# Kernel optimization log

Hardware: AMD Instinct MI355X
Metric: run time of the kernel (lower is better)

The kernel has to match this reference:

```python
import jax, jax.numpy as jnp
import numpy as np


def setup_inputs() -> dict:
    key = jax.random.key(0)
    k1, k2 = jax.random.split(key)
    B, D, T = 8, 256, 4096
    Q, K = 8, 1024
    z = jax.random.normal(k1, (B, D, T), dtype=jnp.float32)
    # original init: uniform(-1/n_e, 1/n_e)
    codebooks = jax.random.uniform(k2, (Q, K, D), dtype=jnp.float32,
                                   minval=-1.0 / K, maxval=1.0 / K)
    return {"z": z, "codebooks": codebooks}


def reference(z, codebooks):
    # z: [B, e_dim, T]; codebooks: [Q, n_e, e_dim]
    zp = jnp.transpose(z, (0, 2, 1))  # [B, T, D]
    residual = zp
    quantized_out = jnp.zeros_like(zp)
    total_loss = jnp.zeros((), dtype=z.dtype)
    all_indices = []
    Q = codebooks.shape[0]
    for q in range(Q):  # small fixed number of residual stages
        E = codebooks[q]  # [K, D]
        # squared euclidean distances: ||r||^2 + ||e||^2 - 2 r.e
        d = (jnp.sum(residual ** 2, axis=-1, keepdims=True)
             + jnp.sum(E ** 2, axis=-1)
             - 2.0 * jnp.einsum('btd,kd->btk', residual, E))  # [B, T, K]
        idx = jnp.argmin(d, axis=-1)  # [B, T]
        z_q = E[idx]                  # [B, T, D] gather
        loss = (jnp.mean((jax.lax.stop_gradient(z_q) - residual) ** 2)
                + 0.25 * jnp.mean((z_q - jax.lax.stop_gradient(residual)) ** 2))
        # straight-through estimator
        z_q_st = residual + jax.lax.stop_gradient(z_q - residual)
        residual = residual - z_q_st
        quantized_out = quantized_out + z_q_st
        total_loss = total_loss + loss
        all_indices.append(idx)
    quantized_out = jnp.transpose(quantized_out, (0, 2, 1))  # [B, D, T]
    return quantized_out, total_loss, jnp.stack(all_indices)  # indices: [Q, B, T]
```

## Files before the change

kernel.cpp:

```cpp
#include <hip/hip_runtime.h>

#define B_   8
#define D_   256
#define T_   4096
#define Q_   8
#define K_   1024
#define BT_  (B_*T_)
#define N_   (B_*T_*D_)
#define LOSS_OFF N_
#define IDX_OFF  (N_+1)
#define ROWS 32

typedef __attribute__((ext_vector_type(8))) short short8;
typedef __attribute__((ext_vector_type(4))) float float4v;

union U4S8 { uint4 u; short8 s; };

__device__ __forceinline__ unsigned short f2bf(float x) {
    unsigned int u = __float_as_uint(x);
    unsigned int r = (u + 0x7FFFu + ((u >> 16) & 1u)) >> 16;
    return (unsigned short)r;
}
__device__ __forceinline__ float bf2f(unsigned short b) {
    return __uint_as_float(((unsigned int)b) << 16);
}
__device__ __forceinline__ unsigned fkey(float f) {
    unsigned u = __float_as_uint(f);
    return (u & 0x80000000u) ? ~u : (u | 0x80000000u);
}
__device__ __forceinline__ float fkeyinv(unsigned k) {
    unsigned u = (k & 0x80000000u) ? (k & 0x7fffffffu) : ~k;
    return __uint_as_float(u);
}


__global__ void k_init(const float* __restrict__ z, float* __restrict__ residual,
                       double* lossAcc) {
    __shared__ float tile[32][33];
    int b  = blockIdx.z;
    int d0 = blockIdx.y * 32;
    int t0 = blockIdx.x * 32;
    int tx = threadIdx.x & 31;
    int ty = threadIdx.x >> 5;
    const float* zb = z + (size_t)b * D_ * T_;
    #pragma unroll
    for (int r = 0; r < 32; r += 8)
        tile[ty + r][tx] = zb[(size_t)(d0 + ty + r) * T_ + t0 + tx];
    __syncthreads();
    float* rb = residual + (size_t)b * T_ * D_;
    #pragma unroll
    for (int r = 0; r < 32; r += 8)
        rb[(size_t)(t0 + ty + r) * D_ + d0 + tx] = tile[tx][ty + r];
    if (b == 0 && blockIdx.x == 0 && blockIdx.y == 0 && threadIdx.x == 0)
        *lossAcc = 0.0;
}


__global__ void k_bfrag(const float* __restrict__ cb, uint4* __restrict__ Bfrag) {
    int gid = blockIdx.x * 256 + threadIdx.x;
    int q    = gid >> 15;
    int rem  = gid & 32767;
    int ct   = rem >> 9;
    int kc   = (rem >> 6) & 7;
    int lane = rem & 63;
    int cand = ct * 16 + (lane & 15);
    int kb   = kc * 32 + (lane >> 4) * 8;
    const float* e = cb + ((size_t)q * K_ + cand) * D_ + kb;
    float4v u0 = *(const float4v*)(e);
    float4v u1 = *(const float4v*)(e + 4);
    float vv[8] = {u0.x, u0.y, u0.z, u0.w, u1.x, u1.y, u1.z, u1.w};
    unsigned short h[8], l[8];
    #pragma unroll
    for (int j = 0; j < 8; ++j) {
        float v = vv[j];
        h[j] = f2bf(v);
        l[j] = f2bf(v - bf2f(h[j]));
    }
    uint4 hi, lo;
    hi.x = (unsigned)h[0] | ((unsigned)h[1] << 16);
    hi.y = (unsigned)h[2] | ((unsigned)h[3] << 16);
    hi.z = (unsigned)h[4] | ((unsigned)h[5] << 16);
    hi.w = (unsigned)h[6] | ((unsigned)h[7] << 16);
    lo.x = (unsigned)l[0] | ((unsigned)l[1] << 16);
    lo.y = (unsigned)l[2] | ((unsigned)l[3] << 16);
    lo.z = (unsigned)l[4] | ((unsigned)l[5] << 16);
    lo.w = (unsigned)l[6] | ((unsigned)l[7] << 16);
    size_t base = (((size_t)(q * 64 + ct) * 8 + kc) * 2) * 64;
    Bfrag[base + lane]      = hi;
    Bfrag[base + 64 + lane] = lo;
}


__global__ void k_se(const float* __restrict__ cb, float* __restrict__ Se) {
    int gid = blockIdx.x * 256 + threadIdx.x;
    int i  = gid >> 4;
    int ln = gid & 15;
    if (i >= Q_ * K_) return;
    const float* e = cb + (size_t)i * D_ + ln * 16;
    float4v v0 = *(const float4v*)(e);
    float4v v1 = *(const float4v*)(e + 4);
    float4v v2 = *(const float4v*)(e + 8);
    float4v v3 = *(const float4v*)(e + 12);
    float vv[16] = {v0.x, v0.y, v0.z, v0.w, v1.x, v1.y, v1.z, v1.w,
                    v2.x, v2.y, v2.z, v2.w, v3.x, v3.y, v3.z, v3.w};
    double s = 0.0;
    #pragma unroll
    for (int d = 0; d < 16; ++d) {
        float a = vv[d] * vv[d];
        s += (double)a;
    }
    #pragma unroll
    for (int st = 8; st > 0; st >>= 1) s += __shfl_xor(s, st);
    if (ln == 0) Se[i] = (float)s;
}


__launch_bounds__(512, 2)
__global__ void k_stage(const float* __restrict__ cb,
                        const uint4* __restrict__ Bfrag,
                        const float* __restrict__ Se,
                        float* __restrict__ residual,
                        float* __restrict__ out,
                        double* __restrict__ lossAcc,
                        int q) {
    __shared__ union {
        uint4 afr[2048];
        struct { int slist[32][16]; float sdd[32][16];
                 int srow[512]; int sslot[512]; } post;
        struct { float ovd[512]; int ovk[512]; } over;
        double lred[8];
    } sc;
    __shared__ float seL[1024];
    __shared__ float srb[32], margin[32];
    __shared__ unsigned sminI[32];
    __shared__ int   scount[32], sidx[32];
    __shared__ int   nSurv;

    const int tid  = threadIdx.x;
    const int lane = tid & 63;
    const int w    = tid >> 6;
    const int quad = lane >> 4;
    const int lc   = lane & 15;
    const int row0 = blockIdx.x * ROWS;
    const int g    = tid >> 8;
    const int dt   = tid & 255;

    if (tid < 32) { scount[tid] = 0; sminI[tid] = 0xFFFFFFFFu; }
    if (tid == 32) nSurv = 0;
    seL[tid]       = Se[q * K_ + tid];
    seL[tid + 512] = Se[q * K_ + tid + 512];

    const uint4* __restrict__ Bq = Bfrag + (size_t)q * (64 * 8 * 2 * 64);
    U4S8 b0h, b0l, b1h, b1l;
    {
        const uint4* p0 = Bq + (((size_t)((w * 8 + 0) * 8 + 0)) * 2) * 64 + lane;
        b0h.u = p0[0]; b0l.u = p0[64];
        const uint4* p1 = Bq + (((size_t)((w * 8 + 1) * 8 + 0)) * 2) * 64 + lane;
        b1h.u = p1[0]; b1l.u = p1[64];
    }

    {
        int row = tid >> 4, seg = tid & 15;
        int rg = row >> 4, rlo = row & 15;
        int kc = seg >> 1, par = seg & 1;
        const float* rp = residual + (size_t)(row0 + row) * D_ + seg * 16;
        float4v v0 = *(const float4v*)(rp);
        float4v v1 = *(const float4v*)(rp + 4);
        float4v v2 = *(const float4v*)(rp + 8);
        float4v v3 = *(const float4v*)(rp + 12);
        float vv[16] = {v0.x, v0.y, v0.z, v0.w, v1.x, v1.y, v1.z, v1.w,
                        v2.x, v2.y, v2.z, v2.w, v3.x, v3.y, v3.z, v3.w};
        double s = 0.0; float sa = 0.0f;
        #pragma unroll
        for (int i = 0; i < 16; ++i) {
            float v = vv[i];
            s += (double)(v * v);
            sa += fabsf(v);
        }
        #pragma unroll
        for (int st = 8; st > 0; st >>= 1) {
            s  += __shfl_xor(s, st);
            sa += __shfl_xor(sa, st);
        }
        if (seg == 0) {
            float sr = (float)s;
            float sb = sa * 1.001f;
            srb[row]    = sr;
            margin[row] = 9.6e-7f * sr + 4.0e-7f * sb + 2.0e-4f;
        }
        #pragma unroll
        for (int h = 0; h < 2; ++h) {
            unsigned short hh[8], ll[8];
            #pragma unroll
            for (int j = 0; j < 8; ++j) {
                float v = vv[h * 8 + j];
                hh[j] = f2bf(v);
                ll[j] = f2bf(v - bf2f(hh[j]));
            }
            uint4 hiW, loW;
            hiW.x = (unsigned)hh[0] | ((unsigned)hh[1] << 16);
            hiW.y = (unsigned)hh[2] | ((unsigned)hh[3] << 16);
            hiW.z = (unsigned)hh[4] | ((unsigned)hh[5] << 16);
            hiW.w = (unsigned)hh[6] | ((unsigned)hh[7] << 16);
            loW.x = (unsigned)ll[0] | ((unsigned)ll[1] << 16);
            loW.y = (unsigned)ll[2] | ((unsigned)ll[3] << 16);
            loW.z = (unsigned)ll[4] | ((unsigned)ll[5] << 16);
            loW.w = (unsigned)ll[6] | ((unsigned)ll[7] << 16);
            int ln = (par * 2 + h) * 16 + rlo;
            int sl = ln ^ kc;
            sc.afr[((rg * 8 + kc) * 2 + 0) * 64 + sl] = hiW;
            sc.afr[((rg * 8 + kc) * 2 + 1) * 64 + sl] = loW;
        }
    }
    __syncthreads();

    float4v accA[16];
    #pragma unroll
    for (int i = 0; i < 16; ++i) accA[i] = (float4v){0.f, 0.f, 0.f, 0.f};

    for (int kc = 0; kc < 8; ++kc) {
        U4S8 a0h, a0l, a1h, a1l;
        a0h.u = sc.afr[((0 * 8 + kc) * 2 + 0) * 64 + (lane ^ kc)];
        a0l.u = sc.afr[((0 * 8 + kc) * 2 + 1) * 64 + (lane ^ kc)];
        a1h.u = sc.afr[((1 * 8 + kc) * 2 + 0) * 64 + (lane ^ kc)];
        a1l.u = sc.afr[((1 * 8 + kc) * 2 + 1) * 64 + (lane ^ kc)];
        #pragma unroll
        for (int ctl = 0; ctl < 8; ++ctl) {
            U4S8 bh, bl;
            if ((ctl & 1) == 0) { bh = b0h; bl = b0l; }
            else                { bh = b1h; bl = b1l; }
            {
                int pkc  = kc + ((ctl + 2) >> 3);
                int pctl = (ctl + 2) & 7;
                const uint4* p = Bq + (((size_t)((w * 8 + pctl) * 8 + pkc)) * 2) * 64 + lane;
                if ((ctl & 1) == 0) { b0h.u = p[0]; b0l.u = p[64]; }
                else                { b1h.u = p[0]; b1l.u = p[64]; }
            }
            float4v a0 = accA[ctl * 2 + 0];
            a0 = __builtin_amdgcn_mfma_f32_16x16x32_bf16(a0h.s, bh.s, a0, 0, 0, 0);
            a0 = __builtin_amdgcn_mfma_f32_16x16x32_bf16(a0l.s, bh.s, a0, 0, 0, 0);
            a0 = __builtin_amdgcn_mfma_f32_16x16x32_bf16(a0h.s, bl.s, a0, 0, 0, 0);
            accA[ctl * 2 + 0] = a0;
            float4v a1 = accA[ctl * 2 + 1];
            a1 = __builtin_amdgcn_mfma_f32_16x16x32_bf16(a1h.s, bh.s, a1, 0, 0, 0);
            a1 = __builtin_amdgcn_mfma_f32_16x16x32_bf16(a1l.s, bh.s, a1, 0, 0, 0);
            a1 = __builtin_amdgcn_mfma_f32_16x16x32_bf16(a1h.s, bl.s, a1, 0, 0, 0);
            accA[ctl * 2 + 1] = a1;
        }
    }

    float sr8[8];
    #pragma unroll
    for (int rr = 0; rr < 8; ++rr)
        sr8[rr] = srb[(rr >> 2) * 16 + quad * 4 + (rr & 3)];

    float mn[8];
    #pragma unroll
    for (int rr = 0; rr < 8; ++rr) mn[rr] = 3.4e38f;
    #pragma unroll
    for (int ctl = 0; ctl < 8; ++ctl) {
        int cand = (w * 8 + ctl) * 16 + lc;
        float se = seL[cand];
        #pragma unroll
        for (int rr = 0; rr < 8; ++rr) {
            float dd = (sr8[rr] + se) - 2.0f * accA[ctl * 2 + (rr >> 2)][rr & 3];
            mn[rr] = fminf(mn[rr], dd);
        }
    }
    #pragma unroll
    for (int rr = 0; rr < 8; ++rr) {
        float v = mn[rr];
        v = fminf(v, __shfl_xor(v, 1));
        v = fminf(v, __shfl_xor(v, 2));
        v = fminf(v, __shfl_xor(v, 4));
        v = fminf(v, __shfl_xor(v, 8));
        if (lc == 0)
            atomicMin(&sminI[(rr >> 2) * 16 + quad * 4 + (rr & 3)], fkey(v));
    }
    __syncthreads();

    float thrV[8];
    #pragma unroll
    for (int rr = 0; rr < 8; ++rr) {
        int row = (rr >> 2) * 16 + quad * 4 + (rr & 3);
        thrV[rr] = fkeyinv(sminI[row]) + margin[row];
    }
    #pragma unroll
    for (int ctl = 0; ctl < 8; ++ctl) {
        int cand = (w * 8 + ctl) * 16 + lc;
        float se = seL[cand];
        #pragma unroll
        for (int rr = 0; rr < 8; ++rr) {
            int row = (rr >> 2) * 16 + quad * 4 + (rr & 3);
            float dd = (sr8[rr] + se) - 2.0f * accA[ctl * 2 + (rr >> 2)][rr & 3];
            if (dd <= thrV[rr]) {
                int p = atomicAdd(&scount[row], 1);
                if (p < 16) sc.post.slist[row][p] = cand;
            }
        }
    }
    __syncthreads();

    if (tid < 32) {
        int cnt = scount[tid];
        if (cnt == 1) {
            sidx[tid] = sc.post.slist[tid][0];
        } else if (cnt >= 2 && cnt <= 16) {
            int base = atomicAdd(&nSurv, cnt);
            for (int s2 = 0; s2 < cnt; ++s2) {
                sc.post.srow[base + s2]  = tid;
                sc.post.sslot[base + s2] = s2;
            }
        }
    }
    __syncthreads();

    {
        int nS  = nSurv;
        int grp = tid >> 4, ln = tid & 15;
        for (int j = grp; j < nS; j += 32) {
            int row  = sc.post.srow[j];
            int slot = sc.post.sslot[j];
            int k    = sc.post.slist[row][slot];
            const float* Ek = cb + ((size_t)q * K_ + k) * D_ + ln * 16;
            const float* Rk = residual + (size_t)(row0 + row) * D_ + ln * 16;
            float4v e0 = *(const float4v*)(Ek);
            float4v e1 = *(const float4v*)(Ek + 4);
            float4v e2 = *(const float4v*)(Ek + 8);
            float4v e3 = *(const float4v*)(Ek + 12);
            float4v r0 = *(const float4v*)(Rk);
            float4v r1 = *(const float4v*)(Rk + 4);
            float4v r2 = *(const float4v*)(Rk + 8);
            float4v r3 = *(const float4v*)(Rk + 12);
            float ev[16] = {e0.x, e0.y, e0.z, e0.w, e1.x, e1.y, e1.z, e1.w,
                            e2.x, e2.y, e2.z, e2.w, e3.x, e3.y, e3.z, e3.w};
            float rv2[16] = {r0.x, r0.y, r0.z, r0.w, r1.x, r1.y, r1.z, r1.w,
                             r2.x, r2.y, r2.z, r2.w, r3.x, r3.y, r3.z, r3.w};
            double a0 = 0.0, a1 = 0.0;
            #pragma unroll
            for (int d = 0; d < 16; d += 2) {
                a0 = fma((double)ev[d],     (double)rv2[d],     a0);
                a1 = fma((double)ev[d + 1], (double)rv2[d + 1], a1);
            }
            double ssum = a0 + a1;
            #pragma unroll
            for (int st = 8; st > 0; st >>= 1) ssum += __shfl_xor(ssum, st);
            if (ln == 0) {
                float dotf = (float)ssum;
                float V = srb[row] + seL[k];
                sc.post.sdd[row][slot] = V - 2.0f * dotf;
            }
        }
    }
    __syncthreads();
    if (tid < 32) {
        int cnt = scount[tid];
        if (cnt >= 2 && cnt <= 16) {
            float bd = 3.4e38f; int bk = 0x7fffffff;
            for (int s2 = 0; s2 < cnt; ++s2) {
                float dv = sc.post.sdd[tid][s2]; int kv = sc.post.slist[tid][s2];
                if (dv < bd || (dv == bd && kv < bk)) { bd = dv; bk = kv; }
            }
            sidx[tid] = bk;
        }
    }
    __syncthreads();

    for (int row = 0; row < ROWS; ++row) {
        int cnt = scount[row];
        if (cnt <= 16) continue;
        const float* Rr = residual + (size_t)(row0 + row) * D_;
        float bd = 3.4e38f; int bk = K_;
        #pragma unroll
        for (int c = 0; c < 2; ++c) {
            int k = tid * 2 + c;
            const float* Ek = cb + ((size_t)q * K_ + k) * D_;
            double a0 = 0.0, a1 = 0.0;
            for (int d = 0; d < D_; d += 2) {
                a0 = fma((double)Ek[d],     (double)Rr[d],     a0);
                a1 = fma((double)Ek[d + 1], (double)Rr[d + 1], a1);
            }
            float dd = (srb[row] + seL[k]) - 2.0f * (float)(a0 + a1);
            if (dd < bd || (dd == bd && k < bk)) { bd = dd; bk = k; }
        }
        sc.over.ovd[tid] = bd; sc.over.ovk[tid] = bk;
        __syncthreads();
        for (int st = 256; st > 0; st >>= 1) {
            if (tid < st) {
                float od = sc.over.ovd[tid + st]; int ok = sc.over.ovk[tid + st];
                if (od < sc.over.ovd[tid] ||
                    (od == sc.over.ovd[tid] && ok < sc.over.ovk[tid])) {
                    sc.over.ovd[tid] = od; sc.over.ovk[tid] = ok;
                }
            }
            __syncthreads();
        }
        if (tid == 0) sidx[row] = sc.over.ovk[0];
        __syncthreads();
    }

    const float* Eq = cb + (size_t)q * K_ * D_;
    double lsum = 0.0;
    #pragma unroll
    for (int jj = 0; jj < 16; ++jj) {
        int row = g * 16 + jj;
        int idx = sidx[row];
        size_t roff = (size_t)(row0 + row) * D_ + dt;
        float rv   = residual[roff];
        float zq   = Eq[(size_t)idx * D_ + dt];
        float t1   = zq - rv;
        float zqst = rv + t1;
        residual[roff] = rv - zqst;
        lsum += (double)t1 * (double)t1;
    }
    if (tid < 32) out[IDX_OFF + q * BT_ + row0 + tid] = (float)sidx[tid];

    #pragma unroll
    for (int st = 32; st > 0; st >>= 1) lsum += __shfl_xor(lsum, st);
    __syncthreads();
    if (lane == 0) sc.lred[w] = lsum;
    __syncthreads();
    if (tid == 0) {
        double t = 0.0;
        #pragma unroll
        for (int i = 0; i < 8; ++i) t += sc.lred[i];
        atomicAdd(lossAcc, t);
    }
}


__global__ void k_emit(const float* __restrict__ z, const float* __restrict__ residual,
                       float* __restrict__ out) {
    __shared__ float tile[32][33];
    int b  = blockIdx.z;
    int t0 = blockIdx.y * 32;
    int d0 = blockIdx.x * 32;
    int tx = threadIdx.x & 31;
    int ty = threadIdx.x >> 5;
    const float* rb = residual + (size_t)b * T_ * D_;
    #pragma unroll
    for (int r = 0; r < 32; r += 8)
        tile[ty + r][tx] = rb[(size_t)(t0 + ty + r) * D_ + d0 + tx];
    __syncthreads();
    const float* zb = z + (size_t)b * D_ * T_;
    float* ob = out + (size_t)b * D_ * T_;
    #pragma unroll
    for (int r = 0; r < 32; r += 8) {
        size_t off = (size_t)(d0 + ty + r) * T_ + t0 + tx;
        ob[off] = zb[off] - tile[tx][ty + r];
    }
}

__global__ void k_final(const double* lossAcc, float* out) {
    if (threadIdx.x == 0 && blockIdx.x == 0) {
        double m = *lossAcc / (double)N_;
        out[LOSS_OFF] = (float)(1.25 * m);
    }
}


extern "C" void kernel_launch(void* const* d_in, const int* in_sizes, int n_in,
                              void* d_out, int out_size, void* d_ws, size_t ws_size,
                              hipStream_t stream) {
    const float* z  = (const float*)d_in[0];
    const float* cb = (const float*)d_in[1];
    float* out = (float*)d_out;

    float*  residual = (float*)d_ws;
    uint4*  Bfrag    = (uint4*)((char*)d_ws + (size_t)N_ * 4);
    float*  Se       = (float*)((char*)d_ws + (size_t)N_ * 4 + (size_t)8 * 1024 * 1024);
    double* lossAcc  = (double*)((char*)d_ws + (size_t)N_ * 4 + (size_t)8 * 1024 * 1024
                                 + (size_t)Q_ * K_ * 4);

    hipLaunchKernelGGL(k_init, dim3(T_ / 32, D_ / 32, B_), dim3(256), 0, stream,
                       z, residual, lossAcc);
    hipLaunchKernelGGL(k_bfrag, dim3(1024), dim3(256), 0, stream, cb, Bfrag);
    hipLaunchKernelGGL(k_se, dim3((Q_ * K_ * 16 + 255) / 256), dim3(256), 0, stream,
                       cb, Se);
    for (int q = 0; q < Q_; ++q) {
        hipLaunchKernelGGL(k_stage, dim3(BT_ / ROWS), dim3(512), 0, stream,
                           cb, Bfrag, Se, residual, out, lossAcc, q);
    }
    hipLaunchKernelGGL(k_emit, dim3(D_ / 32, T_ / 32, B_), dim3(256), 0, stream,
                       z, residual, out);
    hipLaunchKernelGGL(k_final, dim3(1), dim3(256), 0, stream, lossAcc, out);
}
```

Baseline: 818.0 us.

## Fuse all quantizer stages into one kernel with residual held in LDS

Replaces the eight per-stage launches with a single persistent kernel per 32-row block that loops over the stages. The residual tile is loaded into shared memory once, updated in place each stage, and written back to global memory only at the end. This removes the residual round trips through global memory and the per-stage launch gaps. In exchange it adds about 33KB of LDS per block, which may cut occupancy below the two blocks per CU that the launch bounds ask for, and it loses the overlap between stages that separate launches gave.

```diff
diff --git a/kernel.cpp b/kernel.cpp
--- a/kernel.cpp
+++ b/kernel.cpp
@@ -10,6 +10,7 @@
 #define LOSS_OFF N_
 #define IDX_OFF  (N_+1)
 #define ROWS 32
+#define RP   260
 
 typedef __attribute__((ext_vector_type(8))) short short8;
 typedef __attribute__((ext_vector_type(4))) float float4v;
@@ -116,13 +117,13 @@
 
 
 __launch_bounds__(512, 2)
-__global__ void k_stage(const float* __restrict__ cb,
-                        const uint4* __restrict__ Bfrag,
-                        const float* __restrict__ Se,
-                        float* __restrict__ residual,
-                        float* __restrict__ out,
-                        double* __restrict__ lossAcc,
-                        int q) {
+__global__ void k_stages(const float* __restrict__ cb,
+                         const uint4* __restrict__ Bfrag,
+                         const float* __restrict__ Se,
+                         float* __restrict__ residual,
+                         float* __restrict__ out,
+                         double* __restrict__ lossAcc) {
+    __shared__ float r32[ROWS][RP];
     __shared__ union {
         uint4 afr[2048];
         struct { int slist[32][16]; float sdd[32][16];
@@ -145,279 +146,294 @@
     const int g    = tid >> 8;
     const int dt   = tid & 255;
 
-    if (tid < 32) { scount[tid] = 0; sminI[tid] = 0xFFFFFFFFu; }
-    if (tid == 32) nSurv = 0;
-    seL[tid]       = Se[q * K_ + tid];
-    seL[tid + 512] = Se[q * K_ + tid + 512];
-
-    const uint4* __restrict__ Bq = Bfrag + (size_t)q * (64 * 8 * 2 * 64);
-    U4S8 b0h, b0l, b1h, b1l;
-    {
-        const uint4* p0 = Bq + (((size_t)((w * 8 + 0) * 8 + 0)) * 2) * 64 + lane;
-        b0h.u = p0[0]; b0l.u = p0[64];
-        const uint4* p1 = Bq + (((size_t)((w * 8 + 1) * 8 + 0)) * 2) * 64 + lane;
-        b1h.u = p1[0]; b1l.u = p1[64];
-    }
-
-    {
-        int row = tid >> 4, seg = tid & 15;
-        int rg = row >> 4, rlo = row & 15;
-        int kc = seg >> 1, par = seg & 1;
-        const float* rp = residual + (size_t)(row0 + row) * D_ + seg * 16;
-        float4v v0 = *(const float4v*)(rp);
-        float4v v1 = *(const float4v*)(rp + 4);
-        float4v v2 = *(const float4v*)(rp + 8);
-        float4v v3 = *(const float4v*)(rp + 12);
-        float vv[16] = {v0.x, v0.y, v0.z, v0.w, v1.x, v1.y, v1.z, v1.w,
-                        v2.x, v2.y, v2.z, v2.w, v3.x, v3.y, v3.z, v3.w};
-        double s = 0.0; float sa = 0.0f;
-        #pragma unroll
-        for (int i = 0; i < 16; ++i) {
-            float v = vv[i];
-            s += (double)(v * v);
-            sa += fabsf(v);
-        }
-        #pragma unroll
-        for (int st = 8; st > 0; st >>= 1) {
-            s  += __shfl_xor(s, st);
-            sa += __shfl_xor(sa, st);
-        }
-        if (seg == 0) {
-            float sr = (float)s;
-            float sb = sa * 1.001f;
-            srb[row]    = sr;
-            margin[row] = 9.6e-7f * sr + 4.0e-7f * sb + 2.0e-4f;
-        }
-        #pragma unroll
-        for (int h = 0; h < 2; ++h) {
-            unsigned short hh[8], ll[8];
-            #pragma unroll
-            for (int j = 0; j < 8; ++j) {
-                float v = vv[h * 8 + j];
-                hh[j] = f2bf(v);
-                ll[j] = f2bf(v - bf2f(hh[j]));
-            }
-            uint4 hiW, loW;
-            hiW.x = (unsigned)hh[0] | ((unsigned)hh[1] << 16);
-            hiW.y = (unsigned)hh[2] | ((unsigned)hh[3] << 16);
-            hiW.z = (unsigned)hh[4] | ((unsigned)hh[5] << 16);
-            hiW.w = (unsigned)hh[6] | ((unsigned)hh[7] << 16);
-            loW.x = (unsigned)ll[0] | ((unsigned)ll[1] << 16);
-            loW.y = (unsigned)ll[2] | ((unsigned)ll[3] << 16);
-            loW.z = (unsigned)ll[4] | ((unsigned)ll[5] << 16);
-            loW.w = (unsigned)ll[6] | ((unsigned)ll[7] << 16);
-            int ln = (par * 2 + h) * 16 + rlo;
-            int sl = ln ^ kc;
-            sc.afr[((rg * 8 + kc) * 2 + 0) * 64 + sl] = hiW;
-            sc.afr[((rg * 8 + kc) * 2 + 1) * 64 + sl] = loW;
-        }
+    #pragma unroll
+    for (int jj = 0; jj < 16; ++jj) {
+        int row = g * 16 + jj;
+        r32[row][dt] = residual[(size_t)(row0 + row) * D_ + dt];
     }
     __syncthreads();
 
-    float4v accA[16];
-    #pragma unroll
-    for (int i = 0; i < 16; ++i) accA[i] = (float4v){0.f, 0.f, 0.f, 0.f};
-
-    for (int kc = 0; kc < 8; ++kc) {
-        U4S8 a0h, a0l, a1h, a1l;
-        a0h.u = sc.afr[((0 * 8 + kc) * 2 + 0) * 64 + (lane ^ kc)];
-        a0l.u = sc.afr[((0 * 8 + kc) * 2 + 1) * 64 + (lane ^ kc)];
-        a1h.u = sc.afr[((1 * 8 + kc) * 2 + 0) * 64 + (lane ^ kc)];
-        a1l.u = sc.afr[((1 * 8 + kc) * 2 + 1) * 64 + (lane ^ kc)];
+    double lsum = 0.0;
+
+    for (int q = 0; q < Q_; ++q) {
+        if (tid < 32) { scount[tid] = 0; sminI[tid] = 0xFFFFFFFFu; }
+        if (tid == 32) nSurv = 0;
+        seL[tid]       = Se[q * K_ + tid];
+        seL[tid + 512] = Se[q * K_ + tid + 512];
+
+        const uint4* __restrict__ Bq = Bfrag + (size_t)q * (64 * 8 * 2 * 64);
+        U4S8 b0h, b0l, b1h, b1l;
+        {
+            const uint4* p0 = Bq + (((size_t)((w * 8 + 0) * 8 + 0)) * 2) * 64 + lane;
+            b0h.u = p0[0]; b0l.u = p0[64];
+            const uint4* p1 = Bq + (((size_t)((w * 8 + 1) * 8 + 0)) * 2) * 64 + lane;
+            b1h.u = p1[0]; b1l.u = p1[64];
+        }
+
+        {
+            int row = tid >> 4, seg = tid & 15;
+            int rg = row >> 4, rlo = row & 15;
+            int kc = seg >> 1, par = seg & 1;
+            const float* rp = &r32[row][seg * 16];
+            float4v v0 = *(const float4v*)(rp);
+            float4v v1 = *(const float4v*)(rp + 4);
+            float4v v2 = *(const float4v*)(rp + 8);
+            float4v v3 = *(const float4v*)(rp + 12);
+            float vv[16] = {v0.x, v0.y, v0.z, v0.w, v1.x, v1.y, v1.z, v1.w,
+                            v2.x, v2.y, v2.z, v2.w, v3.x, v3.y, v3.z, v3.w};
+            double s = 0.0; float sa = 0.0f;
+            #pragma unroll
+            for (int i = 0; i < 16; ++i) {
+                float v = vv[i];
+                s += (double)(v * v);
+                sa += fabsf(v);
+            }
+            #pragma unroll
+            for (int st = 8; st > 0; st >>= 1) {
+                s  += __shfl_xor(s, st);
+                sa += __shfl_xor(sa, st);
+            }
+            if (seg == 0) {
+                float sr = (float)s;
+                float sb = sa * 1.001f;
+                srb[row]    = sr;
+                margin[row] = 9.6e-7f * sr + 4.0e-7f * sb + 2.0e-4f;
+            }
+            #pragma unroll
+            for (int h = 0; h < 2; ++h) {
+                unsigned short hh[8], ll[8];
+                #pragma unroll
+                for (int j = 0; j < 8; ++j) {
+                    float v = vv[h * 8 + j];
+                    hh[j] = f2bf(v);
+                    ll[j] = f2bf(v - bf2f(hh[j]));
+                }
+                uint4 hiW, loW;
+                hiW.x = (unsigned)hh[0] | ((unsigned)hh[1] << 16);
+                hiW.y = (unsigned)hh[2] | ((unsigned)hh[3] << 16);
+                hiW.z = (unsigned)hh[4] | ((unsigned)hh[5] << 16);
+                hiW.w = (unsigned)hh[6] | ((unsigned)hh[7] << 16);
+                loW.x = (unsigned)ll[0] | ((unsigned)ll[1] << 16);
+                loW.y = (unsigned)ll[2] | ((unsigned)ll[3] << 16);
+                loW.z = (unsigned)ll[4] | ((unsigned)ll[5] << 16);
+                loW.w = (unsigned)ll[6] | ((unsigned)ll[7] << 16);
+                int ln = (par * 2 + h) * 16 + rlo;
+                int sl = ln ^ kc;
+                sc.afr[((rg * 8 + kc) * 2 + 0) * 64 + sl] = hiW;
+                sc.afr[((rg * 8 + kc) * 2 + 1) * 64 + sl] = loW;
+            }
+        }
+        __syncthreads();
+
+        float4v accA[16];
+        #pragma unroll
+        for (int i = 0; i < 16; ++i) accA[i] = (float4v){0.f, 0.f, 0.f, 0.f};
+
+        for (int kc = 0; kc < 8; ++kc) {
+            U4S8 a0h, a0l, a1h, a1l;
+            a0h.u = sc.afr[((0 * 8 + kc) * 2 + 0) * 64 + (lane ^ kc)];
+            a0l.u = sc.afr[((0 * 8 + kc) * 2 + 1) * 64 + (lane ^ kc)];
+            a1h.u = sc.afr[((1 * 8 + kc) * 2 + 0) * 64 + (lane ^ kc)];
+            a1l.u = sc.afr[((1 * 8 + kc) * 2 + 1) * 64 + (lane ^ kc)];
+            #pragma unroll
+            for (int ctl = 0; ctl < 8; ++ctl) {
+                U4S8 bh, bl;
+                if ((ctl & 1) == 0) { bh = b0h; bl = b0l; }
+                else                { bh = b1h; bl = b1l; }
+                {
+                    int pkc  = kc + ((ctl + 2) >> 3);
+                    int pctl = (ctl + 2) & 7;
+                    const uint4* p = Bq + (((size_t)((w * 8 + pctl) * 8 + pkc)) * 2) * 64 + lane;
+                    if ((ctl & 1) == 0) { b0h.u = p[0]; b0l.u = p[64]; }
+                    else                { b1h.u = p[0]; b1l.u = p[64]; }
+                }
+                float4v a0 = accA[ctl * 2 + 0];
+                a0 = __builtin_amdgcn_mfma_f32_16x16x32_bf16(a0h.s, bh.s, a0, 0, 0, 0);
+                a0 = __builtin_amdgcn_mfma_f32_16x16x32_bf16(a0l.s, bh.s, a0, 0, 0, 0);
+                a0 = __builtin_amdgcn_mfma_f32_16x16x32_bf16(a0h.s, bl.s, a0, 0, 0, 0);
+                accA[ctl * 2 + 0] = a0;
+                float4v a1 = accA[ctl * 2 + 1];
+                a1 = __builtin_amdgcn_mfma_f32_16x16x32_bf16(a1h.s, bh.s, a1, 0, 0, 0);
+                a1 = __builtin_amdgcn_mfma_f32_16x16x32_bf16(a1l.s, bh.s, a1, 0, 0, 0);
+                a1 = __builtin_amdgcn_mfma_f32_16x16x32_bf16(a1h.s, bl.s, a1, 0, 0, 0);
+                accA[ctl * 2 + 1] = a1;
+            }
+        }
+
+        float sr8[8];
+        #pragma unroll
+        for (int rr = 0; rr < 8; ++rr)
+            sr8[rr] = srb[(rr >> 2) * 16 + quad * 4 + (rr & 3)];
+
+        float mn[8];
+        #pragma unroll
+        for (int rr = 0; rr < 8; ++rr) mn[rr] = 3.4e38f;
         #pragma unroll
         for (int ctl = 0; ctl < 8; ++ctl) {
-            U4S8 bh, bl;
-            if ((ctl & 1) == 0) { bh = b0h; bl = b0l; }
-            else                { bh = b1h; bl = b1l; }
-            {
-                int pkc  = kc + ((ctl + 2) >> 3);
-                int pctl = (ctl + 2) & 7;
-                const uint4* p = Bq + (((size_t)((w * 8 + pctl) * 8 + pkc)) * 2) * 64 + lane;
-                if ((ctl & 1) == 0) { b0h.u = p[0]; b0l.u = p[64]; }
-                else                { b1h.u = p[0]; b1l.u = p[64]; }
-            }
-            float4v a0 = accA[ctl * 2 + 0];
-            a0 = __builtin_amdgcn_mfma_f32_16x16x32_bf16(a0h.s, bh.s, a0, 0, 0, 0);
-            a0 = __builtin_amdgcn_mfma_f32_16x16x32_bf16(a0l.s, bh.s, a0, 0, 0, 0);
-            a0 = __builtin_amdgcn_mfma_f32_16x16x32_bf16(a0h.s, bl.s, a0, 0, 0, 0);
-            accA[ctl * 2 + 0] = a0;
-            float4v a1 = accA[ctl * 2 + 1];
-            a1 = __builtin_amdgcn_mfma_f32_16x16x32_bf16(a1h.s, bh.s, a1, 0, 0, 0);
-            a1 = __builtin_amdgcn_mfma_f32_16x16x32_bf16(a1l.s, bh.s, a1, 0, 0, 0);
-            a1 = __builtin_amdgcn_mfma_f32_16x16x32_bf16(a1h.s, bl.s, a1, 0, 0, 0);
-            accA[ctl * 2 + 1] = a1;
-        }
-    }
-
-    float sr8[8];
-    #pragma unroll
-    for (int rr = 0; rr < 8; ++rr)
-        sr8[rr] = srb[(rr >> 2) * 16 + quad * 4 + (rr & 3)];
-
-    float mn[8];
-    #pragma unroll
-    for (int rr = 0; rr < 8; ++rr) mn[rr] = 3.4e38f;
-    #pragma unroll
-    for (int ctl = 0; ctl < 8; ++ctl) {
-        int cand = (w * 8 + ctl) * 16 + lc;
-        float se = seL[cand];
+            int cand = (w * 8 + ctl) * 16 + lc;
+            float se = seL[cand];
+            #pragma unroll
+            for (int rr = 0; rr < 8; ++rr) {
+                float dd = (sr8[rr] + se) - 2.0f * accA[ctl * 2 + (rr >> 2)][rr & 3];
+                mn[rr] = fminf(mn[rr], dd);
+            }
+        }
         #pragma unroll
         for (int rr = 0; rr < 8; ++rr) {
-            float dd = (sr8[rr] + se) - 2.0f * accA[ctl * 2 + (rr >> 2)][rr & 3];
-            mn[rr] = fminf(mn[rr], dd);
-        }
-    }
-    #pragma unroll
-    for (int rr = 0; rr < 8; ++rr) {
-        float v = mn[rr];
-        v = fminf(v, __shfl_xor(v, 1));
-        v = fminf(v, __shfl_xor(v, 2));
-        v = fminf(v, __shfl_xor(v, 4));
-        v = fminf(v, __shfl_xor(v, 8));
-        if (lc == 0)
-            atomicMin(&sminI[(rr >> 2) * 16 + quad * 4 + (rr & 3)], fkey(v));
-    }
-    __syncthreads();
-
-    float thrV[8];
-    #pragma unroll
-    for (int rr = 0; rr < 8; ++rr) {
-        int row = (rr >> 2) * 16 + quad * 4 + (rr & 3);
-        thrV[rr] = fkeyinv(sminI[row]) + margin[row];
-    }
-    #pragma unroll
-    for (int ctl = 0; ctl < 8; ++ctl) {
-        int cand = (w * 8 + ctl) * 16 + lc;
-        float se = seL[cand];
+            float v = mn[rr];
+            v = fminf(v, __shfl_xor(v, 1));
+            v = fminf(v, __shfl_xor(v, 2));
+            v = fminf(v, __shfl_xor(v, 4));
+            v = fminf(v, __shfl_xor(v, 8));
+            if (lc == 0)
+                atomicMin(&sminI[(rr >> 2) * 16 + quad * 4 + (rr & 3)], fkey(v));
+        }
+        __syncthreads();
+
+        float thrV[8];
         #pragma unroll
         for (int rr = 0; rr < 8; ++rr) {
             int row = (rr >> 2) * 16 + quad * 4 + (rr & 3);
-            float dd = (sr8[rr] + se) - 2.0f * accA[ctl * 2 + (rr >> 2)][rr & 3];
-            if (dd <= thrV[rr]) {
-                int p = atomicAdd(&scount[row], 1);
-                if (p < 16) sc.post.slist[row][p] = cand;
-            }
-        }
-    }
-    __syncthreads();
-
-    if (tid < 32) {
-        int cnt = scount[tid];
-        if (cnt == 1) {
-            sidx[tid] = sc.post.slist[tid][0];
-        } else if (cnt >= 2 && cnt <= 16) {
-            int base = atomicAdd(&nSurv, cnt);
-            for (int s2 = 0; s2 < cnt; ++s2) {
-                sc.post.srow[base + s2]  = tid;
-                sc.post.sslot[base + s2] = s2;
-            }
-        }
-    }
-    __syncthreads();
-
-    {
-        int nS  = nSurv;
-        int grp = tid >> 4, ln = tid & 15;
-        for (int j = grp; j < nS; j += 32) {
-            int row  = sc.post.srow[j];
-            int slot = sc.post.sslot[j];
-            int k    = sc.post.slist[row][slot];
-            const float* Ek = cb + ((size_t)q * K_ + k) * D_ + ln * 16;
-            const float* Rk = residual + (size_t)(row0 + row) * D_ + ln * 16;
-            float4v e0 = *(const float4v*)(Ek);
-            float4v e1 = *(const float4v*)(Ek + 4);
-            float4v e2 = *(const float4v*)(Ek + 8);
-            float4v e3 = *(const float4v*)(Ek + 12);
-            float4v r0 = *(const float4v*)(Rk);
-            float4v r1 = *(const float4v*)(Rk + 4);
-            float4v r2 = *(const float4v*)(Rk + 8);
-            float4v r3 = *(const float4v*)(Rk + 12);
-            float ev[16] = {e0.x, e0.y, e0.z, e0.w, e1.x, e1.y, e1.z, e1.w,
-                            e2.x, e2.y, e2.z, e2.w, e3.x, e3.y, e3.z, e3.w};
-            float rv2[16] = {r0.x, r0.y, r0.z, r0.w, r1.x, r1.y, r1.z, r1.w,
-                             r2.x, r2.y, r2.z, r2.w, r3.x, r3.y, r3.z, r3.w};
-            double a0 = 0.0, a1 = 0.0;
-            #pragma unroll
-            for (int d = 0; d < 16; d += 2) {
-                a0 = fma((double)ev[d],     (double)rv2[d],     a0);
-                a1 = fma((double)ev[d + 1], (double)rv2[d + 1], a1);
-            }
-            double ssum = a0 + a1;
-            #pragma unroll
-            for (int st = 8; st > 0; st >>= 1) ssum += __shfl_xor(ssum, st);
-            if (ln == 0) {
-                float dotf = (float)ssum;
-                float V = srb[row] + seL[k];
-                sc.post.sdd[row][slot] = V - 2.0f * dotf;
-            }
-        }
-    }
-    __syncthreads();
-    if (tid < 32) {
-        int cnt = scount[tid];
-        if (cnt >= 2 && cnt <= 16) {
-            float bd = 3.4e38f; int bk = 0x7fffffff;
-            for (int s2 = 0; s2 < cnt; ++s2) {
-                float dv = sc.post.sdd[tid][s2]; int kv = sc.post.slist[tid][s2];
-                if (dv < bd || (dv == bd && kv < bk)) { bd = dv; bk = kv; }
-            }
-            sidx[tid] = bk;
-        }
-    }
-    __syncthreads();
-
-    for (int row = 0; row < ROWS; ++row) {
-        int cnt = scount[row];
-        if (cnt <= 16) continue;
-        const float* Rr = residual + (size_t)(row0 + row) * D_;
-        float bd = 3.4e38f; int bk = K_;
-        #pragma unroll
-        for (int c = 0; c < 2; ++c) {
-            int k = tid * 2 + c;
-            const float* Ek = cb + ((size_t)q * K_ + k) * D_;
-            double a0 = 0.0, a1 = 0.0;
-            for (int d = 0; d < D_; d += 2) {
-                a0 = fma((double)Ek[d],     (double)Rr[d],     a0);
-                a1 = fma((double)Ek[d + 1], (double)Rr[d + 1], a1);
-            }
-            float dd = (srb[row] + seL[k]) - 2.0f * (float)(a0 + a1);
-            if (dd < bd || (dd == bd && k < bk)) { bd = dd; bk = k; }
-        }
-        sc.over.ovd[tid] = bd; sc.over.ovk[tid] = bk;
-        __syncthreads();
-        for (int st = 256; st > 0; st >>= 1) {
-            if (tid < st) {
-                float od = sc.over.ovd[tid + st]; int ok = sc.over.ovk[tid + st];
-                if (od < sc.over.ovd[tid] ||
-                    (od == sc.over.ovd[tid] && ok < sc.over.ovk[tid])) {
-                    sc.over.ovd[tid] = od; sc.over.ovk[tid] = ok;
-                }
-            }
+            thrV[rr] = fkeyinv(sminI[row]) + margin[row];
+        }
+        #pragma unroll
+        for (int ctl = 0; ctl < 8; ++ctl) {
+            int cand = (w * 8 + ctl) * 16 + lc;
+            float se = seL[cand];
+            #pragma unroll
+            for (int rr = 0; rr < 8; ++rr) {
+                int row = (rr >> 2) * 16 + quad * 4 + (rr & 3);
+                float dd = (sr8[rr] + se) - 2.0f * accA[ctl * 2 + (rr >> 2)][rr & 3];
+                if (dd <= thrV[rr]) {
+                    int p = atomicAdd(&scount[row], 1);
+                    if (p < 16) sc.post.slist[row][p] = cand;
+                }
+            }
+        }
+        __syncthreads();
+
+        if (tid < 32) {
+            int cnt = scount[tid];
+            if (cnt == 1) {
+                sidx[tid] = sc.post.slist[tid][0];
+            } else if (cnt >= 2 && cnt <= 16) {
+                int base = atomicAdd(&nSurv, cnt);
+                for (int s2 = 0; s2 < cnt; ++s2) {
+                    sc.post.srow[base + s2]  = tid;
+                    sc.post.sslot[base + s2] = s2;
+                }
+            }
+        }
+        __syncthreads();
+
+        {
+            int nS  = nSurv;
+            int grp = tid >> 4, ln = tid & 15;
+            for (int j = grp; j < nS; j += 32) {
+                int row  = sc.post.srow[j];
+                int slot = sc.post.sslot[j];
+                int k    = sc.post.slist[row][slot];
+                const float* Ek = cb + ((size_t)q * K_ + k) * D_ + ln * 16;
+                const float* Rk = &r32[row][ln * 16];
+                float4v e0 = *(const float4v*)(Ek);
+                float4v e1 = *(const float4v*)(Ek + 4);
+                float4v e2 = *(const float4v*)(Ek + 8);
+                float4v e3 = *(const float4v*)(Ek + 12);
+                float4v r0 = *(const float4v*)(Rk);
+                float4v r1 = *(const float4v*)(Rk + 4);
+                float4v r2 = *(const float4v*)(Rk + 8);
+                float4v r3 = *(const float4v*)(Rk + 12);
+                float ev[16] = {e0.x, e0.y, e0.z, e0.w, e1.x, e1.y, e1.z, e1.w,
+                                e2.x, e2.y, e2.z, e2.w, e3.x, e3.y, e3.z, e3.w};
+                float rv2[16] = {r0.x, r0.y, r0.z, r0.w, r1.x, r1.y, r1.z, r1.w,
+                                 r2.x, r2.y, r2.z, r2.w, r3.x, r3.y, r3.z, r3.w};
+                double a0 = 0.0, a1 = 0.0;
+                #pragma unroll
+                for (int d = 0; d < 16; d += 2) {
+                    a0 = fma((double)ev[d],     (double)rv2[d],     a0);
+                    a1 = fma((double)ev[d + 1], (double)rv2[d + 1], a1);
+                }
+                double ssum = a0 + a1;
+                #pragma unroll
+                for (int st = 8; st > 0; st >>= 1) ssum += __shfl_xor(ssum, st);
+                if (ln == 0) {
+                    float dotf = (float)ssum;
+                    float V = srb[row] + seL[k];
+                    sc.post.sdd[row][slot] = V - 2.0f * dotf;
+                }
+            }
+        }
+        __syncthreads();
+        if (tid < 32) {
+            int cnt = scount[tid];
+            if (cnt >= 2 && cnt <= 16) {
+                float bd = 3.4e38f; int bk = 0x7fffffff;
+                for (int s2 = 0; s2 < cnt; ++s2) {
+                    float dv = sc.post.sdd[tid][s2]; int kv = sc.post.slist[tid][s2];
+                    if (dv < bd || (dv == bd && kv < bk)) { bd = dv; bk = kv; }
+                }
+                sidx[tid] = bk;
+            }
+        }
+        __syncthreads();
+
+        for (int row = 0; row < ROWS; ++row) {
+            int cnt = scount[row];
+            if (cnt <= 16) continue;
+            float bd = 3.4e38f; int bk = K_;
+            #pragma unroll
+            for (int c = 0; c < 2; ++c) {
+                int k = tid * 2 + c;
+                const float* Ek = cb + ((size_t)q * K_ + k) * D_;
+                double a0 = 0.0, a1 = 0.0;
+                for (int d = 0; d < D_; d += 2) {
+                    a0 = fma((double)Ek[d],     (double)r32[row][d],     a0);
+                    a1 = fma((double)Ek[d + 1], (double)r32[row][d + 1], a1);
+                }
+                float dd = (srb[row] + seL[k]) - 2.0f * (float)(a0 + a1);
+                if (dd < bd || (dd == bd && k < bk)) { bd = dd; bk = k; }
+            }
+            sc.over.ovd[tid] = bd; sc.over.ovk[tid] = bk;
             __syncthreads();
-        }
-        if (tid == 0) sidx[row] = sc.over.ovk[0];
-        __syncthreads();
-    }
-
-    const float* Eq = cb + (size_t)q * K_ * D_;
-    double lsum = 0.0;
+            for (int st = 256; st > 0; st >>= 1) {
+                if (tid < st) {
+                    float od = sc.over.ovd[tid + st]; int ok = sc.over.ovk[tid + st];
+                    if (od < sc.over.ovd[tid] ||
+                        (od == sc.over.ovd[tid] && ok < sc.over.ovk[tid])) {
+                        sc.over.ovd[tid] = od; sc.over.ovk[tid] = ok;
+                    }
+                }
+                __syncthreads();
+            }
+            if (tid == 0) sidx[row] = sc.over.ovk[0];
+            __syncthreads();
+        }
+
+        const float* Eq = cb + (size_t)q * K_ * D_;
+        #pragma unroll
+        for (int jj = 0; jj < 16; ++jj) {
+            int row = g * 16 + jj;
+            int idx = sidx[row];
+            float rv   = r32[row][dt];
+            float zq   = Eq[(size_t)idx * D_ + dt];
+            float t1   = zq - rv;
+            float zqst = rv + t1;
+            r32[row][dt] = rv - zqst;
+            lsum += (double)t1 * (double)t1;
+        }
+        if (tid < 32) out[IDX_OFF + q * BT_ + row0 + tid] = (float)sidx[tid];
+
+        __syncthreads();
+    }
+
     #pragma unroll
     for (int jj = 0; jj < 16; ++jj) {
         int row = g * 16 + jj;
-        int idx = sidx[row];
-        size_t roff = (size_t)(row0 + row) * D_ + dt;
-        float rv   = residual[roff];
-        float zq   = Eq[(size_t)idx * D_ + dt];
-        float t1   = zq - rv;
-        float zqst = rv + t1;
-        residual[roff] = rv - zqst;
-        lsum += (double)t1 * (double)t1;
-    }
-    if (tid < 32) out[IDX_OFF + q * BT_ + row0 + tid] = (float)sidx[tid];
+        residual[(size_t)(row0 + row) * D_ + dt] = r32[row][dt];
+    }
 
     #pragma unroll
     for (int st = 32; st > 0; st >>= 1) lsum += __shfl_xor(lsum, st);
-    __syncthreads();
     if (lane == 0) sc.lred[w] = lsum;
     __syncthreads();
     if (tid == 0) {
@@ -477,10 +493,8 @@
     hipLaunchKernelGGL(k_bfrag, dim3(1024), dim3(256), 0, stream, cb, Bfrag);
     hipLaunchKernelGGL(k_se, dim3((Q_ * K_ * 16 + 255) / 256), dim3(256), 0, stream,
                        cb, Se);
-    for (int q = 0; q < Q_; ++q) {
-        hipLaunchKernelGGL(k_stage, dim3(BT_ / ROWS), dim3(512), 0, stream,
-                           cb, Bfrag, Se, residual, out, lossAcc, q);
-    }
+    hipLaunchKernelGGL(k_stages, dim3(BT_ / ROWS), dim3(512), 0, stream,
+                       cb, Bfrag, Se, residual, out, lossAcc);
     hipLaunchKernelGGL(k_emit, dim3(D_ / 32, T_ / 32, B_), dim3(256), 0, stream,
                        z, residual, out);
     hipLaunchKernelGGL(k_final, dim3(1), dim3(256), 0, stream, lossAcc, out);
```

New measurement: 975.6 us. 19.3% more time.

## Double rows per block to 64 with 1024 threads, halving codebook fragment reloads

Applied to the files above, without the earlier changes.

Each k_stage block now handles 64 rows with 1024 threads (16 waves) instead of 32 rows with 512. Each wave covers 4 codeword column tiles across 4 row groups, so every B fragment loaded from global is reused over twice as many rows. The goal is to halve the codebook fragment traffic per row. In exchange, occupancy drops to one large block per CU, and the per-candidate threshold is now reloaded from shared memory inside the loop.

```diff
diff --git a/kernel.cpp b/kernel.cpp
--- a/kernel.cpp
+++ b/kernel.cpp
@@ -9,7 +9,8 @@
 #define N_   (B_*T_*D_)
 #define LOSS_OFF N_
 #define IDX_OFF  (N_+1)
-#define ROWS 32
+#define ROWS 64
+#define THREADS 1024
 
 typedef __attribute__((ext_vector_type(8))) short short8;
 typedef __attribute__((ext_vector_type(4))) float float4v;
@@ -115,7 +116,7 @@
 }
 
 
-__launch_bounds__(512, 2)
+__launch_bounds__(THREADS, 1)
 __global__ void k_stage(const float* __restrict__ cb,
                         const uint4* __restrict__ Bfrag,
                         const float* __restrict__ Se,
@@ -124,16 +125,16 @@
                         double* __restrict__ lossAcc,
                         int q) {
     __shared__ union {
-        uint4 afr[2048];
-        struct { int slist[32][16]; float sdd[32][16];
-                 int srow[512]; int sslot[512]; } post;
-        struct { float ovd[512]; int ovk[512]; } over;
-        double lred[8];
+        uint4 afr[4096];
+        struct { int slist[64][16]; float sdd[64][16];
+                 int srow[1024]; int sslot[1024]; } post;
+        struct { float ovd[1024]; int ovk[1024]; } over;
+        double lred[16];
     } sc;
     __shared__ float seL[1024];
-    __shared__ float srb[32], margin[32];
-    __shared__ unsigned sminI[32];
-    __shared__ int   scount[32], sidx[32];
+    __shared__ float srb[64], margin[64];
+    __shared__ unsigned sminI[64];
+    __shared__ int   scount[64], sidx[64];
     __shared__ int   nSurv;
 
     const int tid  = threadIdx.x;
@@ -145,18 +146,18 @@
     const int g    = tid >> 8;
     const int dt   = tid & 255;
 
-    if (tid < 32) { scount[tid] = 0; sminI[tid] = 0xFFFFFFFFu; }
-    if (tid == 32) nSurv = 0;
-    seL[tid]       = Se[q * K_ + tid];
-    seL[tid + 512] = Se[q * K_ + tid + 512];
+    if (tid < 64) { scount[tid] = 0; sminI[tid] = 0xFFFFFFFFu; }
+    if (tid == 64) nSurv = 0;
+    seL[tid] = Se[q * K_ + tid];
 
     const uint4* __restrict__ Bq = Bfrag + (size_t)q * (64 * 8 * 2 * 64);
-    U4S8 b0h, b0l, b1h, b1l;
-    {
-        const uint4* p0 = Bq + (((size_t)((w * 8 + 0) * 8 + 0)) * 2) * 64 + lane;
-        b0h.u = p0[0]; b0l.u = p0[64];
-        const uint4* p1 = Bq + (((size_t)((w * 8 + 1) * 8 + 0)) * 2) * 64 + lane;
-        b1h.u = p1[0]; b1l.u = p1[64];
+    U4S8 bh0[2], bl0[2], bh1[2], bl1[2];
+    #pragma unroll
+    for (int c = 0; c < 2; ++c) {
+        const uint4* p0 = Bq + (((size_t)((w * 4 + c) * 8 + 0)) * 2) * 64 + lane;
+        bh0[c].u = p0[0]; bl0[c].u = p0[64];
+        const uint4* p1 = Bq + (((size_t)((w * 4 + 2 + c) * 8 + 0)) * 2) * 64 + lane;
+        bh1[c].u = p1[0]; bl1[c].u = p1[64];
     }
 
     {
@@ -218,57 +219,59 @@
     #pragma unroll
     for (int i = 0; i < 16; ++i) accA[i] = (float4v){0.f, 0.f, 0.f, 0.f};
 
-    for (int kc = 0; kc < 8; ++kc) {
-        U4S8 a0h, a0l, a1h, a1l;
-        a0h.u = sc.afr[((0 * 8 + kc) * 2 + 0) * 64 + (lane ^ kc)];
-        a0l.u = sc.afr[((0 * 8 + kc) * 2 + 1) * 64 + (lane ^ kc)];
-        a1h.u = sc.afr[((1 * 8 + kc) * 2 + 0) * 64 + (lane ^ kc)];
-        a1l.u = sc.afr[((1 * 8 + kc) * 2 + 1) * 64 + (lane ^ kc)];
-        #pragma unroll
-        for (int ctl = 0; ctl < 8; ++ctl) {
-            U4S8 bh, bl;
-            if ((ctl & 1) == 0) { bh = b0h; bl = b0l; }
-            else                { bh = b1h; bl = b1l; }
-            {
-                int pkc  = kc + ((ctl + 2) >> 3);
-                int pctl = (ctl + 2) & 7;
-                const uint4* p = Bq + (((size_t)((w * 8 + pctl) * 8 + pkc)) * 2) * 64 + lane;
-                if ((ctl & 1) == 0) { b0h.u = p[0]; b0l.u = p[64]; }
-                else                { b1h.u = p[0]; b1l.u = p[64]; }
-            }
-            float4v a0 = accA[ctl * 2 + 0];
-            a0 = __builtin_amdgcn_mfma_f32_16x16x32_bf16(a0h.s, bh.s, a0, 0, 0, 0);
-            a0 = __builtin_amdgcn_mfma_f32_16x16x32_bf16(a0l.s, bh.s, a0, 0, 0, 0);
-            a0 = __builtin_amdgcn_mfma_f32_16x16x32_bf16(a0h.s, bl.s, a0, 0, 0, 0);
-            accA[ctl * 2 + 0] = a0;
-            float4v a1 = accA[ctl * 2 + 1];
-            a1 = __builtin_amdgcn_mfma_f32_16x16x32_bf16(a1h.s, bh.s, a1, 0, 0, 0);
-            a1 = __builtin_amdgcn_mfma_f32_16x16x32_bf16(a1l.s, bh.s, a1, 0, 0, 0);
-            a1 = __builtin_amdgcn_mfma_f32_16x16x32_bf16(a1h.s, bl.s, a1, 0, 0, 0);
-            accA[ctl * 2 + 1] = a1;
-        }
-    }
-
-    float sr8[8];
-    #pragma unroll
-    for (int rr = 0; rr < 8; ++rr)
-        sr8[rr] = srb[(rr >> 2) * 16 + quad * 4 + (rr & 3)];
-
-    float mn[8];
-    #pragma unroll
-    for (int rr = 0; rr < 8; ++rr) mn[rr] = 3.4e38f;
-    #pragma unroll
-    for (int ctl = 0; ctl < 8; ++ctl) {
-        int cand = (w * 8 + ctl) * 16 + lc;
+    for (int s = 0; s < 16; ++s) {
+        int kc = s >> 1;
+        int cb0 = (s & 1) * 2;
+        U4S8 bh[2], bl[2];
+        if ((s & 1) == 0) { bh[0] = bh0[0]; bl[0] = bl0[0]; bh[1] = bh0[1]; bl[1] = bl0[1]; }
+        else              { bh[0] = bh1[0]; bl[0] = bl1[0]; bh[1] = bh1[1]; bl[1] = bl1[1]; }
+        {
+            int ps  = (s + 2 > 15) ? 15 : (s + 2);
+            int pkc = ps >> 1;
+            int pc0 = (ps & 1) * 2;
+            #pragma unroll
+            for (int c = 0; c < 2; ++c) {
+                const uint4* p = Bq + (((size_t)((w * 4 + pc0 + c) * 8 + pkc)) * 2) * 64 + lane;
+                if ((s & 1) == 0) { bh0[c].u = p[0]; bl0[c].u = p[64]; }
+                else              { bh1[c].u = p[0]; bl1[c].u = p[64]; }
+            }
+        }
+        #pragma unroll
+        for (int rg = 0; rg < 4; ++rg) {
+            U4S8 ah, al;
+            ah.u = sc.afr[((rg * 8 + kc) * 2 + 0) * 64 + (lane ^ kc)];
+            al.u = sc.afr[((rg * 8 + kc) * 2 + 1) * 64 + (lane ^ kc)];
+            #pragma unroll
+            for (int c = 0; c < 2; ++c) {
+                float4v a = accA[(cb0 + c) * 4 + rg];
+                a = __builtin_amdgcn_mfma_f32_16x16x32_bf16(ah.s, bh[c].s, a, 0, 0, 0);
+                a = __builtin_amdgcn_mfma_f32_16x16x32_bf16(al.s, bh[c].s, a, 0, 0, 0);
+                a = __builtin_amdgcn_mfma_f32_16x16x32_bf16(ah.s, bl[c].s, a, 0, 0, 0);
+                accA[(cb0 + c) * 4 + rg] = a;
+            }
+        }
+    }
+
+    float sr16[16];
+    #pragma unroll
+    for (int rr = 0; rr < 16; ++rr)
+        sr16[rr] = srb[(rr >> 2) * 16 + quad * 4 + (rr & 3)];
+
+    float mn[16];
+    #pragma unroll
+    for (int rr = 0; rr < 16; ++rr) mn[rr] = 3.4e38f;
+    #pragma unroll
+    for (int c = 0; c < 4; ++c) {
+        int cand = (w * 4 + c) * 16 + lc;
         float se = seL[cand];
         #pragma unroll
-        for (int rr = 0; rr < 8; ++rr) {
-            float dd = (sr8[rr] + se) - 2.0f * accA[ctl * 2 + (rr >> 2)][rr & 3];
+        for (int rr = 0; rr < 16; ++rr) {
+            float dd = (sr16[rr] + se) - 2.0f * accA[c * 4 + (rr >> 2)][rr & 3];
             mn[rr] = fminf(mn[rr], dd);
         }
     }
     #pragma unroll
-    for (int rr = 0; rr < 8; ++rr) {
+    for (int rr = 0; rr < 16; ++rr) {
         float v = mn[rr];
         v = fminf(v, __shfl_xor(v, 1));
         v = fminf(v, __shfl_xor(v, 2));
@@ -279,21 +282,16 @@
     }
     __syncthreads();
 
-    float thrV[8];
-    #pragma unroll
-    for (int rr = 0; rr < 8; ++rr) {
-        int row = (rr >> 2) * 16 + quad * 4 + (rr & 3);
-        thrV[rr] = fkeyinv(sminI[row]) + margin[row];
-    }
-    #pragma unroll
-    for (int ctl = 0; ctl < 8; ++ctl) {
-        int cand = (w * 8 + ctl) * 16 + lc;
+    #pragma unroll
+    for (int c = 0; c < 4; ++c) {
+        int cand = (w * 4 + c) * 16 + lc;
         float se = seL[cand];
         #pragma unroll
-        for (int rr = 0; rr < 8; ++rr) {
+        for (int rr = 0; rr < 16; ++rr) {
             int row = (rr >> 2) * 16 + quad * 4 + (rr & 3);
-            float dd = (sr8[rr] + se) - 2.0f * accA[ctl * 2 + (rr >> 2)][rr & 3];
-            if (dd <= thrV[rr]) {
+            float dd = (sr16[rr] + se) - 2.0f * accA[c * 4 + (rr >> 2)][rr & 3];
+            float thr = fkeyinv(sminI[row]) + margin[row];
+            if (dd <= thr) {
                 int p = atomicAdd(&scount[row], 1);
                 if (p < 16) sc.post.slist[row][p] = cand;
             }
@@ -301,7 +299,7 @@
     }
     __syncthreads();
 
-    if (tid < 32) {
+    if (tid < 64) {
         int cnt = scount[tid];
         if (cnt == 1) {
             sidx[tid] = sc.post.slist[tid][0];
@@ -318,7 +316,7 @@
     {
         int nS  = nSurv;
         int grp = tid >> 4, ln = tid & 15;
-        for (int j = grp; j < nS; j += 32) {
+        for (int j = grp; j < nS; j += 64) {
             int row  = sc.post.srow[j];
             int slot = sc.post.sslot[j];
             int k    = sc.post.slist[row][slot];
@@ -353,7 +351,7 @@
         }
     }
     __syncthreads();
-    if (tid < 32) {
+    if (tid < 64) {
         int cnt = scount[tid];
         if (cnt >= 2 && cnt <= 16) {
             float bd = 3.4e38f; int bk = 0x7fffffff;
@@ -370,22 +368,17 @@
         int cnt = scount[row];
         if (cnt <= 16) continue;
         const float* Rr = residual + (size_t)(row0 + row) * D_;
-        float bd = 3.4e38f; int bk = K_;
-        #pragma unroll
-        for (int c = 0; c < 2; ++c) {
-            int k = tid * 2 + c;
-            const float* Ek = cb + ((size_t)q * K_ + k) * D_;
-            double a0 = 0.0, a1 = 0.0;
-            for (int d = 0; d < D_; d += 2) {
-                a0 = fma((double)Ek[d],     (double)Rr[d],     a0);
-                a1 = fma((double)Ek[d + 1], (double)Rr[d + 1], a1);
-            }
-            float dd = (srb[row] + seL[k]) - 2.0f * (float)(a0 + a1);
-            if (dd < bd || (dd == bd && k < bk)) { bd = dd; bk = k; }
-        }
-        sc.over.ovd[tid] = bd; sc.over.ovk[tid] = bk;
+        int k = tid;
+        const float* Ek = cb + ((size_t)q * K_ + k) * D_;
+        double a0 = 0.0, a1 = 0.0;
+        for (int d = 0; d < D_; d += 2) {
+            a0 = fma((double)Ek[d],     (double)Rr[d],     a0);
+            a1 = fma((double)Ek[d + 1], (double)Rr[d + 1], a1);
+        }
+        float bd = (srb[row] + seL[k]) - 2.0f * (float)(a0 + a1);
+        sc.over.ovd[tid] = bd; sc.over.ovk[tid] = k;
         __syncthreads();
-        for (int st = 256; st > 0; st >>= 1) {
+        for (int st = 512; st > 0; st >>= 1) {
             if (tid < st) {
                 float od = sc.over.ovd[tid + st]; int ok = sc.over.ovk[tid + st];
                 if (od < sc.over.ovd[tid] ||
@@ -413,7 +406,7 @@
         residual[roff] = rv - zqst;
         lsum += (double)t1 * (double)t1;
     }
-    if (tid < 32) out[IDX_OFF + q * BT_ + row0 + tid] = (float)sidx[tid];
+    if (tid < 64) out[IDX_OFF + q * BT_ + row0 + tid] = (float)sidx[tid];
 
     #pragma unroll
     for (int st = 32; st > 0; st >>= 1) lsum += __shfl_xor(lsum, st);
@@ -423,7 +416,7 @@
     if (tid == 0) {
         double t = 0.0;
         #pragma unroll
-        for (int i = 0; i < 8; ++i) t += sc.lred[i];
+        for (int i = 0; i < 16; ++i) t += sc.lred[i];
         atomicAdd(lossAcc, t);
     }
 }
@@ -478,7 +471,7 @@
     hipLaunchKernelGGL(k_se, dim3((Q_ * K_ * 16 + 255) / 256), dim3(256), 0, stream,
                        cb, Se);
     for (int q = 0; q < Q_; ++q) {
-        hipLaunchKernelGGL(k_stage, dim3(BT_ / ROWS), dim3(512), 0, stream,
+        hipLaunchKernelGGL(k_stage, dim3(BT_ / ROWS), dim3(THREADS), 0, stream,
                            cb, Bfrag, Se, residual, out, lossAcc, q);
     }
     hipLaunchKernelGGL(k_emit, dim3(D_ / 32, T_ / 32, B_), dim3(256), 0, stream,
```

Result: faster. 781.1 us (-4.5%).
